# Kernel tuning notes

Hardware: AMD Instinct MI355X
Metric: run time of the kernel (lower is better)

## Reference

```python
import jax, jax.numpy as jnp
import numpy as np

B, T, C = 4, 2048, 1024
NH = 16
HD = C // NH  # 64


def setup_inputs() -> dict:
    key = jax.random.key(0)
    k1, k2, k3, k4, k5 = jax.random.split(key, 5)
    s_in = 1.0 / np.sqrt(C)
    return {
        "x": jax.random.normal(k1, (B, T, C), dtype=jnp.float32),
        "attention_mask": jnp.ones((B, T), dtype=jnp.float32),
        "W_qkv": jax.random.normal(k2, (C, 3 * C), dtype=jnp.float32) * s_in,
        "b_qkv": jnp.zeros((3 * C,), dtype=jnp.float32),
        "W_out": jax.random.normal(k3, (C, C), dtype=jnp.float32) * s_in,
        "b_out": jnp.zeros((C,), dtype=jnp.float32),
    }


def reference(x, attention_mask, W_qkv, b_qkv, W_out, b_out):
    Bx, Tx, Cx = x.shape
    # QKV projection: (B,T,3C)
    qkv = x @ W_qkv + b_qkv
    Q, K, V = jnp.split(qkv, 3, axis=-1)
    # (B, NH, T, HD)
    Q = Q.reshape(Bx, Tx, NH, HD).transpose(0, 2, 1, 3)
    K = K.reshape(Bx, Tx, NH, HD).transpose(0, 2, 1, 3)
    V = V.reshape(Bx, Tx, NH, HD).transpose(0, 2, 1, 3)
    # scaled scores (B, NH, T, T)
    scores = jnp.einsum("bhqd,bhkd->bhqk", Q, K) * (1.0 / np.sqrt(HD))
    # causal mask: set strictly-upper triangle to -inf (mask-fill semantics)
    causal = jnp.tril(jnp.ones((Tx, Tx), dtype=bool))[None, None]
    scores = jnp.where(causal, scores, -jnp.inf)
    # additive padding mask
    pad = (1.0 - attention_mask)[:, None, None, :] * jnp.finfo(scores.dtype).min
    scores = scores + pad
    attn = jax.nn.softmax(scores, axis=-1)
    # weighted values -> (B, T, C)
    wv = jnp.einsum("bhqk,bhkd->bhqd", attn, V)
    wv = wv.transpose(0, 2, 1, 3).reshape(Bx, Tx, Cx)
    return wv @ W_out + b_out
```

## Files before the change

kernel.cpp:

```cpp
#include <hip/hip_runtime.h>
#include <math.h>

constexpr int BB = 4;
constexpr int TT = 2048;
constexpr int CC = 1024;
constexpr int NHH = 16;
constexpr int HDD = 64;
constexpr int C3 = 3 * CC;

typedef __bf16 bf16x8 __attribute__((ext_vector_type(8)));
typedef float  f32x4  __attribute__((ext_vector_type(4)));

__device__ __forceinline__ unsigned short f2bf(float x) {
    union { float f; unsigned u; } v; v.f = x;
    unsigned r = v.u + 0x7fffu + ((v.u >> 16) & 1u);
    return (unsigned short)(r >> 16);
}

#define AS1(p) ((const __attribute__((address_space(1))) void*)(p))
#define AS3(p) ((__attribute__((address_space(3))) void*)(p))

constexpr float SM2 = 17.312340490667561f;

constexpr int CAST_BLOCKS = (BB * TT * CC / 4) / 256;
constexpr int TQKV_BLOCKS = (C3 / 64) * (CC / 64);
constexpr int TOUT_BLOCKS = (CC / 64) * (CC / 64);
constexpr int KB_BLOCKS   = (BB * TT) / 256;

__global__ __launch_bounds__(256) void prep(
    const float* __restrict__ x,
    const float* __restrict__ Wqkv,
    const float* __restrict__ Wout,
    const float* __restrict__ amask,
    unsigned short* __restrict__ xb,
    unsigned short* __restrict__ Wqkvt,
    unsigned short* __restrict__ Woutt,
    float* __restrict__ kbias)
{
    __shared__ float tile[64][65];
    const int bid = blockIdx.x;
    const int t = threadIdx.x;

    if (bid < CAST_BLOCKS) {
        const int i = bid * 256 + t;
        float4 v = ((const float4*)x)[i];
        ushort4 o;
        o.x = f2bf(v.x); o.y = f2bf(v.y); o.z = f2bf(v.z); o.w = f2bf(v.w);
        ((ushort4*)xb)[i] = o;
        return;
    }
    if (bid >= CAST_BLOCKS + TQKV_BLOCKS + TOUT_BLOCKS) {
        const int i = (bid - CAST_BLOCKS - TQKV_BLOCKS - TOUT_BLOCKS) * 256 + t;
        kbias[i] = (amask[i] - 1.0f) * 1.0e38f - SM2;
        return;
    }

    const float* src; unsigned short* dst; int R, Cn, r0, c0;
    if (bid < CAST_BLOCKS + TQKV_BLOCKS) {
        const int tb = bid - CAST_BLOCKS;
        src = Wqkv; dst = Wqkvt; R = CC; Cn = C3;
        c0 = (tb % (C3 / 64)) * 64; r0 = (tb / (C3 / 64)) * 64;
    } else {
        const int tb = bid - CAST_BLOCKS - TQKV_BLOCKS;
        src = Wout; dst = Woutt; R = CC; Cn = CC;
        c0 = (tb % (CC / 64)) * 64; r0 = (tb / (CC / 64)) * 64;
    }

    const int lr = t >> 4, lc = (t & 15) * 4;
    #pragma unroll
    for (int s = 0; s < 4; ++s) {
        float4 v = *(const float4*)&src[(size_t)(r0 + lr + s * 16) * Cn + c0 + lc];
        tile[lr + s * 16][lc + 0] = v.x;
        tile[lr + s * 16][lc + 1] = v.y;
        tile[lr + s * 16][lc + 2] = v.z;
        tile[lr + s * 16][lc + 3] = v.w;
    }
    __syncthreads();
    const int oi = t >> 2, oc = (t & 3) * 16;
    unsigned short buf[16];
    #pragma unroll
    for (int u = 0; u < 16; ++u)
        buf[u] = f2bf(tile[oc + u][oi]);
    unsigned short* d = &dst[(size_t)(c0 + oi) * R + r0 + oc];
    *(uint4*)(d + 0) = *(uint4*)&buf[0];
    *(uint4*)(d + 8) = *(uint4*)&buf[8];
}

template<bool VSPLIT>
__global__ __launch_bounds__(256) void gemm_bt_mfma(
    const unsigned short* __restrict__ A,
    const unsigned short* __restrict__ Bt,
    const float* __restrict__ bias,
    float* __restrict__ OutF,
    unsigned short* __restrict__ Qp,
    unsigned short* __restrict__ Kp,
    unsigned short* __restrict__ Vtp,
    int M, int N, int K, float qscale)
{
    __shared__ alignas(16) unsigned short As[128 * 64];
    __shared__ alignas(16) unsigned short Bs[128 * 64];

    const int tid  = threadIdx.x;
    const int w    = tid >> 6;
    const int lane = tid & 63;
    const int quad = lane >> 4;
    const int col  = lane & 15;
    const int m0 = blockIdx.y * 128, n0 = blockIdx.x * 128;
    const int wr = w >> 1, wc = w & 1;

    f32x4 acc[4][4];
    #pragma unroll
    for (int i = 0; i < 4; ++i)
        #pragma unroll
        for (int j = 0; j < 4; ++j)
            #pragma unroll
            for (int r = 0; r < 4; ++r)
                acc[i][j][r] = 0.0f;

    const int srow = tid >> 3;
    const int spos = tid & 7;
    char* AsB = (char*)As;
    char* BsB = (char*)Bs;

    for (int k0 = 0; k0 < K; k0 += 64) {
        if (k0) __syncthreads();
        #pragma unroll
        for (int i = 0; i < 4; ++i) {
            const int row = srow + 32 * i;
            const int sch = spos ^ (row & 7);
            __builtin_amdgcn_global_load_lds(
                AS1(A + (size_t)(m0 + row) * K + k0 + sch * 8),
                AS3(AsB + i * 4096 + w * 1024), 16, 0, 0);
            __builtin_amdgcn_global_load_lds(
                AS1(Bt + (size_t)(n0 + row) * K + k0 + sch * 8),
                AS3(BsB + i * 4096 + w * 1024), 16, 0, 0);
        }
        __syncthreads();

        #pragma unroll
        for (int ks = 0; ks < 2; ++ks) {
            bf16x8 af[4], bf[4];
            #pragma unroll
            for (int i = 0; i < 4; ++i) {
                const int ra = wr * 64 + i * 16 + col;
                const int pa = ((quad + ks * 4) ^ (ra & 7)) * 8;
                af[i] = *(const bf16x8*)&As[ra * 64 + pa];
                const int rb = wc * 64 + i * 16 + col;
                const int pb = ((quad + ks * 4) ^ (rb & 7)) * 8;
                bf[i] = *(const bf16x8*)&Bs[rb * 64 + pb];
            }
            #pragma unroll
            for (int i = 0; i < 4; ++i)
                #pragma unroll
                for (int j = 0; j < 4; ++j)
                    acc[i][j] = __builtin_amdgcn_mfma_f32_16x16x32_bf16(af[i], bf[j], acc[i][j], 0, 0, 0);
        }
    }

    if (VSPLIT) {
        if (n0 < CC) {
            #pragma unroll
            for (int i = 0; i < 4; ++i)
                #pragma unroll
                for (int r = 0; r < 4; ++r) {
                    const int m = m0 + wr * 64 + i * 16 + quad * 4 + r;
                    #pragma unroll
                    for (int j = 0; j < 4; ++j) {
                        const int n = n0 + wc * 64 + j * 16 + col;
                        Qp[(size_t)m * CC + n] = f2bf((acc[i][j][r] + bias[n]) * qscale);
                    }
                }
        } else if (n0 < 2 * CC) {
            #pragma unroll
            for (int i = 0; i < 4; ++i) {
                const int mb   = m0 + wr * 64 + i * 16 + quad * 4;
                const int bidx = mb >> 11;
                const int tloc = mb & 2047;
                #pragma unroll
                for (int j = 0; j < 4; ++j) {
                    const int n  = n0 + wc * 64 + j * 16 + col;
                    const int hh = (n - CC) >> 6;
                    const int dd = (n - CC) & 63;
                    #pragma unroll
                    for (int r = 0; r < 4; ++r)
                        Kp[(((size_t)bidx * NHH + hh) * TT + tloc + r) * HDD + dd] =
                            f2bf(acc[i][j][r] + bias[n]);
                }
            }
        } else {
            #pragma unroll
            for (int i = 0; i < 4; ++i) {
                const int mb   = m0 + wr * 64 + i * 16 + quad * 4;
                const int bidx = mb >> 11;
                const int tloc = mb & 2047;
                const int ktile = tloc >> 6, tc = tloc & 63;
                #pragma unroll
                for (int j = 0; j < 4; ++j) {
                    const int n  = n0 + wc * 64 + j * 16 + col;
                    const int hh = (n - 2 * CC) >> 6;
                    const int dd = (n - 2 * CC) & 63;
                    unsigned short pk[4];
                    #pragma unroll
                    for (int r = 0; r < 4; ++r)
                        pk[r] = f2bf(acc[i][j][r] + bias[n]);
                    *(uint2*)&Vtp[((((size_t)bidx * NHH + hh) * 32 + ktile) * HDD + dd) * 64 + tc] =
                        *(const uint2*)pk;
                }
            }
        }
    } else {
        #pragma unroll
        for (int i = 0; i < 4; ++i)
            #pragma unroll
            for (int r = 0; r < 4; ++r) {
                const int m = m0 + wr * 64 + i * 16 + quad * 4 + r;
                #pragma unroll
                for (int j = 0; j < 4; ++j) {
                    const int n = n0 + wc * 64 + j * 16 + col;
                    OutF[(size_t)m * N + n] = acc[i][j][r] + bias[n];
                }
            }
    }
}

constexpr int PP = 72;

__global__ __launch_bounds__(256, 2) void attn_mfma(
    const unsigned short* __restrict__ Qp,
    const unsigned short* __restrict__ Kp,
    const unsigned short* __restrict__ Vtp,
    const float* __restrict__ kbias,
    unsigned short* __restrict__ WV)
{
    __shared__ alignas(16) unsigned short Ks [2][64 * 64];
    __shared__ alignas(16) unsigned short Vts[2][64 * 64];
    __shared__ alignas(16) __bf16        Ps[4][32 * PP];

    const int tid  = threadIdx.x;
    const int w    = tid >> 6;
    const int lane = tid & 63;
    const int quad = lane >> 4;
    const int col  = lane & 15;

    const int wid = ((blockIdx.x & 7) << 6) | (blockIdx.x >> 3);
    const int bh = wid >> 3, jx = wid & 7;
    const int b = bh >> 4, h = bh & 15;

    const unsigned short* Qg = Qp + (size_t)b * TT * CC + (size_t)h * HDD;
    const unsigned short* Kg = Kp + (size_t)bh * TT * HDD;
    const unsigned short* Vg = Vtp + (size_t)bh * 32 * HDD * 64;
    const float* kb_g = kbias + b * TT;

    const int srow = tid >> 3;
    const int sch  = (tid & 7) ^ (srow & 7);
    char* KsB  = (char*)&Ks[0][0];
    char* VtsB = (char*)&Vts[0][0];

    #pragma unroll
    for (int ph = 0; ph < 2; ++ph) {
        const int qb    = ph ? (15 - jx) : jx;
        const int qbase = qb * 128;
        const int qw    = qbase + w * 32;

        bf16x8 qfa0 = *(const bf16x8*)(Qg + (size_t)(qw + col) * CC + quad * 8);
        bf16x8 qfa1 = *(const bf16x8*)(Qg + (size_t)(qw + col) * CC + 32 + quad * 8);
        bf16x8 qfb0 = *(const bf16x8*)(Qg + (size_t)(qw + 16 + col) * CC + quad * 8);
        bf16x8 qfb1 = *(const bf16x8*)(Qg + (size_t)(qw + 16 + col) * CC + 32 + quad * 8);

        f32x4 o[2][4];
        float l[2][4];
        #pragma unroll
        for (int hh = 0; hh < 2; ++hh)
            #pragma unroll
            for (int t = 0; t < 4; ++t)
                #pragma unroll
                for (int r = 0; r < 4; ++r) o[hh][t][r] = 0.0f;
        #pragma unroll
        for (int hh = 0; hh < 2; ++hh)
            #pragma unroll
            for (int r = 0; r < 4; ++r) l[hh][r] = 0.0f;

        const int ntiles = 2 * qb + 2;

        #pragma unroll
        for (int i = 0; i < 2; ++i) {
            __builtin_amdgcn_global_load_lds(
                AS1(Kg + (size_t)(srow + 32 * i) * HDD + sch * 8),
                AS3(KsB + i * 4096 + w * 1024), 16, 0, 0);
            __builtin_amdgcn_global_load_lds(
                AS1(Vg + (size_t)(srow + 32 * i) * 64 + sch * 8),
                AS3(VtsB + i * 4096 + w * 1024), 16, 0, 0);
        }
        __syncthreads();

        for (int it = 0; it < ntiles; ++it) {
            const int kt  = it << 6;
            const int cur = it & 1;

            if (it + 1 < ntiles) {
                #pragma unroll
                for (int i = 0; i < 2; ++i) {
                    __builtin_amdgcn_global_load_lds(
                        AS1(Kg + (size_t)(kt + 64 + srow + 32 * i) * HDD + sch * 8),
                        AS3(KsB + (cur ^ 1) * 8192 + i * 4096 + w * 1024), 16, 0, 0);
                    __builtin_amdgcn_global_load_lds(
                        AS1(Vg + ((size_t)(it + 1) * 64 + srow + 32 * i) * 64 + sch * 8),
                        AS3(VtsB + (cur ^ 1) * 8192 + i * 4096 + w * 1024), 16, 0, 0);
                }
            }

            if (kt <= qw + 31) {
                const unsigned short* ksb = &Ks[cur][0];
                const unsigned short* vsb = &Vts[cur][0];

                float kb[4];
                #pragma unroll
                for (int t = 0; t < 4; ++t)
                    kb[t] = kb_g[kt + t * 16 + col];

                f32x4 s[2][4];
                #pragma unroll
                for (int t = 0; t < 4; ++t) {
                    const int row = t * 16 + col;
                    const int c0 = (quad ^ (row & 7)) * 8;
                    const int c1 = ((quad + 4) ^ (row & 7)) * 8;
                    bf16x8 k0 = *(const bf16x8*)&ksb[row * 64 + c0];
                    bf16x8 k1 = *(const bf16x8*)&ksb[row * 64 + c1];
                    f32x4 z;
                    #pragma unroll
                    for (int r = 0; r < 4; ++r) z[r] = kb[t];
                    f32x4 za = __builtin_amdgcn_mfma_f32_16x16x32_bf16(qfa0, k0, z, 0, 0, 0);
                    za = __builtin_amdgcn_mfma_f32_16x16x32_bf16(qfa1, k1, za, 0, 0, 0);
                    s[0][t] = za;
                    f32x4 zb = __builtin_amdgcn_mfma_f32_16x16x32_bf16(qfb0, k0, z, 0, 0, 0);
                    zb = __builtin_amdgcn_mfma_f32_16x16x32_bf16(qfb1, k1, zb, 0, 0, 0);
                    s[1][t] = zb;
                }

                const bool needc = (kt + 64 > qw);
                #pragma unroll
                for (int hh = 0; hh < 2; ++hh)
                    #pragma unroll
                    for (int t = 0; t < 4; ++t) {
                        const int key = kt + t * 16 + col;
                        #pragma unroll
                        for (int r = 0; r < 4; ++r) {
                            float p = __builtin_amdgcn_exp2f(s[hh][t][r]);
                            if (needc && key > qw + hh * 16 + quad * 4 + r) p = 0.0f;
                            l[hh][r] += p;
                            Ps[w][(hh * 16 + quad * 4 + r) * PP + t * 16 + col] = (__bf16)p;
                        }
                    }

                bf16x8 p0a = *(const bf16x8*)&Ps[w][col * PP + quad * 8];
                bf16x8 p1a = *(const bf16x8*)&Ps[w][col * PP + 32 + quad * 8];
                bf16x8 p0b = *(const bf16x8*)&Ps[w][(16 + col) * PP + quad * 8];
                bf16x8 p1b = *(const bf16x8*)&Ps[w][(16 + col) * PP + 32 + quad * 8];
                #pragma unroll
                for (int t = 0; t < 4; ++t) {
                    const int row = t * 16 + col;
                    const int c0 = (quad ^ (row & 7)) * 8;
                    const int c1 = ((quad + 4) ^ (row & 7)) * 8;
                    bf16x8 v0 = *(const bf16x8*)&vsb[row * 64 + c0];
                    bf16x8 v1 = *(const bf16x8*)&vsb[row * 64 + c1];
                    o[0][t] = __builtin_amdgcn_mfma_f32_16x16x32_bf16(p0a, v0, o[0][t], 0, 0, 0);
                    o[0][t] = __builtin_amdgcn_mfma_f32_16x16x32_bf16(p1a, v1, o[0][t], 0, 0, 0);
                    o[1][t] = __builtin_amdgcn_mfma_f32_16x16x32_bf16(p0b, v0, o[1][t], 0, 0, 0);
                    o[1][t] = __builtin_amdgcn_mfma_f32_16x16x32_bf16(p1b, v1, o[1][t], 0, 0, 0);
                }
            }
            __syncthreads();
        }

        #pragma unroll
        for (int hh = 0; hh < 2; ++hh) {
            #pragma unroll
            for (int off = 1; off < 16; off <<= 1)
                #pragma unroll
                for (int r = 0; r < 4; ++r)
                    l[hh][r] += __shfl_xor(l[hh][r], off);
            #pragma unroll
            for (int r = 0; r < 4; ++r) {
                const float inv = 1.0f / l[hh][r];
                const int q = qw + hh * 16 + quad * 4 + r;
                unsigned short* dst = WV + ((size_t)b * TT + q) * CC + (size_t)h * HDD;
                #pragma unroll
                for (int t = 0; t < 4; ++t)
                    dst[t * 16 + col] = f2bf(o[hh][t][r] * inv);
            }
        }
    }
}

extern "C" void kernel_launch(void* const* d_in, const int* in_sizes, int n_in,
                              void* d_out, int out_size, void* d_ws, size_t ws_size,
                              hipStream_t stream) {
    const float* x     = (const float*)d_in[0];
    const float* amask = (const float*)d_in[1];
    const float* Wqkv  = (const float*)d_in[2];
    const float* bqkv  = (const float*)d_in[3];
    const float* Wout  = (const float*)d_in[4];
    const float* bout  = (const float*)d_in[5];
    float* out = (float*)d_out;

    const int M = BB * TT;

    unsigned short* xb    = (unsigned short*)d_ws;
    unsigned short* Wqkvt = xb    + (size_t)M * CC;
    unsigned short* Woutt = Wqkvt + (size_t)C3 * CC;
    unsigned short* Qp    = Woutt + (size_t)CC * CC;
    unsigned short* Kp    = Qp    + (size_t)M * CC;
    unsigned short* Vtp   = Kp    + (size_t)M * CC;
    unsigned short* wvb   = Vtp   + (size_t)M * CC;
    float*          kbias = (float*)(wvb + (size_t)M * CC);

    dim3 blk(256);

    prep<<<dim3(CAST_BLOCKS + TQKV_BLOCKS + TOUT_BLOCKS + KB_BLOCKS), blk, 0, stream>>>(
        x, Wqkv, Wout, amask, xb, Wqkvt, Woutt, kbias);

    gemm_bt_mfma<true><<<dim3(C3 / 128, M / 128), blk, 0, stream>>>(
        xb, Wqkvt, bqkv, nullptr, Qp, Kp, Vtp, M, C3, CC, 0.18033688011112043f);
    attn_mfma<<<dim3(512), dim3(256), 0, stream>>>(
        Qp, Kp, Vtp, kbias, wvb);
    gemm_bt_mfma<false><<<dim3(CC / 128, M / 128), blk, 0, stream>>>(
        wvb, Woutt, bout, out, nullptr, nullptr, nullptr, M, CC, CC, 1.0f);
}
```

Before: 257.2 us.

## Split attention into one query block per CTA with depth-2 DMA prefetch

The attention kernel no longer pairs two causal query blocks (jx and 15-jx) per block. It launches 1024 blocks, one query block each, ordered longest-first so the heavy blocks are scheduled early and load balance comes from the hardware scheduler. The K/V pipeline now keeps two tiles in flight, using explicit vmcnt waits and raw s_barrier in place of __syncthreads, and it prefetches key-bias values a tile ahead. Launch bounds are raised to 3 blocks per SM to allow more occupancy. The risks are register pressure at the tighter bound and the hand-written waitcnt counts, which must match the number of DMA and bias loads issued per tile.

```diff
diff --git a/kernel.cpp b/kernel.cpp
--- a/kernel.cpp
+++ b/kernel.cpp
@@ -225,7 +225,7 @@
 
 constexpr int PP = 72;
 
-__global__ __launch_bounds__(256, 2) void attn_mfma(
+__global__ __launch_bounds__(256, 3) void attn_mfma(
     const unsigned short* __restrict__ Qp,
     const unsigned short* __restrict__ Kp,
     const unsigned short* __restrict__ Vtp,
@@ -242,8 +242,10 @@
     const int quad = lane >> 4;
     const int col  = lane & 15;
 
-    const int wid = ((blockIdx.x & 7) << 6) | (blockIdx.x >> 3);
-    const int bh = wid >> 3, jx = wid & 7;
+    const int gi = blockIdx.x;
+    const int j  = gi >> 3;
+    const int bh = ((gi & 7) << 3) | (j & 7);
+    const int qb = 15 - (j >> 3);
     const int b = bh >> 4, h = bh & 15;
 
     const unsigned short* Qg = Qp + (size_t)b * TT * CC + (size_t)h * HDD;
@@ -256,138 +258,141 @@
     char* KsB  = (char*)&Ks[0][0];
     char* VtsB = (char*)&Vts[0][0];
 
-    #pragma unroll
-    for (int ph = 0; ph < 2; ++ph) {
-        const int qb    = ph ? (15 - jx) : jx;
-        const int qbase = qb * 128;
-        const int qw    = qbase + w * 32;
-
-        bf16x8 qfa0 = *(const bf16x8*)(Qg + (size_t)(qw + col) * CC + quad * 8);
-        bf16x8 qfa1 = *(const bf16x8*)(Qg + (size_t)(qw + col) * CC + 32 + quad * 8);
-        bf16x8 qfb0 = *(const bf16x8*)(Qg + (size_t)(qw + 16 + col) * CC + quad * 8);
-        bf16x8 qfb1 = *(const bf16x8*)(Qg + (size_t)(qw + 16 + col) * CC + 32 + quad * 8);
-
-        f32x4 o[2][4];
-        float l[2][4];
-        #pragma unroll
-        for (int hh = 0; hh < 2; ++hh)
-            #pragma unroll
-            for (int t = 0; t < 4; ++t)
-                #pragma unroll
-                for (int r = 0; r < 4; ++r) o[hh][t][r] = 0.0f;
-        #pragma unroll
-        for (int hh = 0; hh < 2; ++hh)
-            #pragma unroll
-            for (int r = 0; r < 4; ++r) l[hh][r] = 0.0f;
-
-        const int ntiles = 2 * qb + 2;
-
+    const int qw = qb * 128 + w * 32;
+    const int ntiles = 2 * qb + 2;
+
+    bf16x8 qfa0 = *(const bf16x8*)(Qg + (size_t)(qw + col) * CC + quad * 8);
+    bf16x8 qfa1 = *(const bf16x8*)(Qg + (size_t)(qw + col) * CC + 32 + quad * 8);
+    bf16x8 qfb0 = *(const bf16x8*)(Qg + (size_t)(qw + 16 + col) * CC + quad * 8);
+    bf16x8 qfb1 = *(const bf16x8*)(Qg + (size_t)(qw + 16 + col) * CC + 32 + quad * 8);
+
+    f32x4 o[2][4];
+    float l[2][4];
+    #pragma unroll
+    for (int hh = 0; hh < 2; ++hh)
+        #pragma unroll
+        for (int t = 0; t < 4; ++t)
+            #pragma unroll
+            for (int r = 0; r < 4; ++r) o[hh][t][r] = 0.0f;
+    #pragma unroll
+    for (int hh = 0; hh < 2; ++hh)
+        #pragma unroll
+        for (int r = 0; r < 4; ++r) l[hh][r] = 0.0f;
+
+    auto DMA = [&](int tile, int buf) {
         #pragma unroll
         for (int i = 0; i < 2; ++i) {
             __builtin_amdgcn_global_load_lds(
-                AS1(Kg + (size_t)(srow + 32 * i) * HDD + sch * 8),
-                AS3(KsB + i * 4096 + w * 1024), 16, 0, 0);
+                AS1(Kg + (size_t)(tile * 64 + srow + 32 * i) * HDD + sch * 8),
+                AS3(KsB + buf * 8192 + i * 4096 + w * 1024), 16, 0, 0);
             __builtin_amdgcn_global_load_lds(
-                AS1(Vg + (size_t)(srow + 32 * i) * 64 + sch * 8),
-                AS3(VtsB + i * 4096 + w * 1024), 16, 0, 0);
-        }
-        __syncthreads();
-
-        for (int it = 0; it < ntiles; ++it) {
-            const int kt  = it << 6;
-            const int cur = it & 1;
-
-            if (it + 1 < ntiles) {
-                #pragma unroll
-                for (int i = 0; i < 2; ++i) {
-                    __builtin_amdgcn_global_load_lds(
-                        AS1(Kg + (size_t)(kt + 64 + srow + 32 * i) * HDD + sch * 8),
-                        AS3(KsB + (cur ^ 1) * 8192 + i * 4096 + w * 1024), 16, 0, 0);
-                    __builtin_amdgcn_global_load_lds(
-                        AS1(Vg + ((size_t)(it + 1) * 64 + srow + 32 * i) * 64 + sch * 8),
-                        AS3(VtsB + (cur ^ 1) * 8192 + i * 4096 + w * 1024), 16, 0, 0);
+                AS1(Vg + ((size_t)tile * 64 + srow + 32 * i) * 64 + sch * 8),
+                AS3(VtsB + buf * 8192 + i * 4096 + w * 1024), 16, 0, 0);
+        }
+    };
+
+    float kbc[4], kbn[4];
+    DMA(0, 0);
+    #pragma unroll
+    for (int t = 0; t < 4; ++t) kbc[t] = kb_g[t * 16 + col];
+    DMA(1, 1);
+    #pragma unroll
+    for (int t = 0; t < 4; ++t) kbn[t] = kb_g[64 + t * 16 + col];
+    asm volatile("s_waitcnt vmcnt(8)" ::: "memory");
+    __builtin_amdgcn_s_barrier();
+
+    for (int it = 0; it < ntiles; ++it) {
+        const int kt  = it << 6;
+        const int cur = it & 1;
+
+        if (kt <= qw + 31) {
+            const unsigned short* ksb = &Ks[cur][0];
+            const unsigned short* vsb = &Vts[cur][0];
+
+            f32x4 s[2][4];
+            #pragma unroll
+            for (int t = 0; t < 4; ++t) {
+                const int row = t * 16 + col;
+                const int c0 = (quad ^ (row & 7)) * 8;
+                const int c1 = ((quad + 4) ^ (row & 7)) * 8;
+                bf16x8 k0 = *(const bf16x8*)&ksb[row * 64 + c0];
+                bf16x8 k1 = *(const bf16x8*)&ksb[row * 64 + c1];
+                f32x4 z;
+                #pragma unroll
+                for (int r = 0; r < 4; ++r) z[r] = kbc[t];
+                f32x4 za = __builtin_amdgcn_mfma_f32_16x16x32_bf16(qfa0, k0, z, 0, 0, 0);
+                za = __builtin_amdgcn_mfma_f32_16x16x32_bf16(qfa1, k1, za, 0, 0, 0);
+                s[0][t] = za;
+                f32x4 zb = __builtin_amdgcn_mfma_f32_16x16x32_bf16(qfb0, k0, z, 0, 0, 0);
+                zb = __builtin_amdgcn_mfma_f32_16x16x32_bf16(qfb1, k1, zb, 0, 0, 0);
+                s[1][t] = zb;
+            }
+
+            const bool needc = (kt + 64 > qw);
+            #pragma unroll
+            for (int hh = 0; hh < 2; ++hh)
+                #pragma unroll
+                for (int t = 0; t < 4; ++t) {
+                    const int key = kt + t * 16 + col;
+                    #pragma unroll
+                    for (int r = 0; r < 4; ++r) {
+                        float p = __builtin_amdgcn_exp2f(s[hh][t][r]);
+                        if (needc && key > qw + hh * 16 + quad * 4 + r) p = 0.0f;
+                        l[hh][r] += p;
+                        Ps[w][(hh * 16 + quad * 4 + r) * PP + t * 16 + col] = (__bf16)p;
+                    }
                 }
-            }
-
-            if (kt <= qw + 31) {
-                const unsigned short* ksb = &Ks[cur][0];
-                const unsigned short* vsb = &Vts[cur][0];
-
-                float kb[4];
-                #pragma unroll
-                for (int t = 0; t < 4; ++t)
-                    kb[t] = kb_g[kt + t * 16 + col];
-
-                f32x4 s[2][4];
-                #pragma unroll
-                for (int t = 0; t < 4; ++t) {
-                    const int row = t * 16 + col;
-                    const int c0 = (quad ^ (row & 7)) * 8;
-                    const int c1 = ((quad + 4) ^ (row & 7)) * 8;
-                    bf16x8 k0 = *(const bf16x8*)&ksb[row * 64 + c0];
-                    bf16x8 k1 = *(const bf16x8*)&ksb[row * 64 + c1];
-                    f32x4 z;
-                    #pragma unroll
-                    for (int r = 0; r < 4; ++r) z[r] = kb[t];
-                    f32x4 za = __builtin_amdgcn_mfma_f32_16x16x32_bf16(qfa0, k0, z, 0, 0, 0);
-                    za = __builtin_amdgcn_mfma_f32_16x16x32_bf16(qfa1, k1, za, 0, 0, 0);
-                    s[0][t] = za;
-                    f32x4 zb = __builtin_amdgcn_mfma_f32_16x16x32_bf16(qfb0, k0, z, 0, 0, 0);
-                    zb = __builtin_amdgcn_mfma_f32_16x16x32_bf16(qfb1, k1, zb, 0, 0, 0);
-                    s[1][t] = zb;
-                }
-
-                const bool needc = (kt + 64 > qw);
-                #pragma unroll
-                for (int hh = 0; hh < 2; ++hh)
-                    #pragma unroll
-                    for (int t = 0; t < 4; ++t) {
-                        const int key = kt + t * 16 + col;
-                        #pragma unroll
-                        for (int r = 0; r < 4; ++r) {
-                            float p = __builtin_amdgcn_exp2f(s[hh][t][r]);
-                            if (needc && key > qw + hh * 16 + quad * 4 + r) p = 0.0f;
-                            l[hh][r] += p;
-                            Ps[w][(hh * 16 + quad * 4 + r) * PP + t * 16 + col] = (__bf16)p;
-                        }
-                    }
-
-                bf16x8 p0a = *(const bf16x8*)&Ps[w][col * PP + quad * 8];
-                bf16x8 p1a = *(const bf16x8*)&Ps[w][col * PP + 32 + quad * 8];
-                bf16x8 p0b = *(const bf16x8*)&Ps[w][(16 + col) * PP + quad * 8];
-                bf16x8 p1b = *(const bf16x8*)&Ps[w][(16 + col) * PP + 32 + quad * 8];
-                #pragma unroll
-                for (int t = 0; t < 4; ++t) {
-                    const int row = t * 16 + col;
-                    const int c0 = (quad ^ (row & 7)) * 8;
-                    const int c1 = ((quad + 4) ^ (row & 7)) * 8;
-                    bf16x8 v0 = *(const bf16x8*)&vsb[row * 64 + c0];
-                    bf16x8 v1 = *(const bf16x8*)&vsb[row * 64 + c1];
-                    o[0][t] = __builtin_amdgcn_mfma_f32_16x16x32_bf16(p0a, v0, o[0][t], 0, 0, 0);
-                    o[0][t] = __builtin_amdgcn_mfma_f32_16x16x32_bf16(p1a, v1, o[0][t], 0, 0, 0);
-                    o[1][t] = __builtin_amdgcn_mfma_f32_16x16x32_bf16(p0b, v0, o[1][t], 0, 0, 0);
-                    o[1][t] = __builtin_amdgcn_mfma_f32_16x16x32_bf16(p1b, v1, o[1][t], 0, 0, 0);
-                }
-            }
-            __syncthreads();
-        }
-
-        #pragma unroll
-        for (int hh = 0; hh < 2; ++hh) {
-            #pragma unroll
-            for (int off = 1; off < 16; off <<= 1)
-                #pragma unroll
-                for (int r = 0; r < 4; ++r)
-                    l[hh][r] += __shfl_xor(l[hh][r], off);
-            #pragma unroll
-            for (int r = 0; r < 4; ++r) {
-                const float inv = 1.0f / l[hh][r];
-                const int q = qw + hh * 16 + quad * 4 + r;
-                unsigned short* dst = WV + ((size_t)b * TT + q) * CC + (size_t)h * HDD;
-                #pragma unroll
-                for (int t = 0; t < 4; ++t)
-                    dst[t * 16 + col] = f2bf(o[hh][t][r] * inv);
-            }
+
+            bf16x8 p0a = *(const bf16x8*)&Ps[w][col * PP + quad * 8];
+            bf16x8 p1a = *(const bf16x8*)&Ps[w][col * PP + 32 + quad * 8];
+            bf16x8 p0b = *(const bf16x8*)&Ps[w][(16 + col) * PP + quad * 8];
+            bf16x8 p1b = *(const bf16x8*)&Ps[w][(16 + col) * PP + 32 + quad * 8];
+            #pragma unroll
+            for (int t = 0; t < 4; ++t) {
+                const int row = t * 16 + col;
+                const int c0 = (quad ^ (row & 7)) * 8;
+                const int c1 = ((quad + 4) ^ (row & 7)) * 8;
+                bf16x8 v0 = *(const bf16x8*)&vsb[row * 64 + c0];
+                bf16x8 v1 = *(const bf16x8*)&vsb[row * 64 + c1];
+                o[0][t] = __builtin_amdgcn_mfma_f32_16x16x32_bf16(p0a, v0, o[0][t], 0, 0, 0);
+                o[0][t] = __builtin_amdgcn_mfma_f32_16x16x32_bf16(p1a, v1, o[0][t], 0, 0, 0);
+                o[1][t] = __builtin_amdgcn_mfma_f32_16x16x32_bf16(p0b, v0, o[1][t], 0, 0, 0);
+                o[1][t] = __builtin_amdgcn_mfma_f32_16x16x32_bf16(p1b, v1, o[1][t], 0, 0, 0);
+            }
+        }
+
+        __builtin_amdgcn_s_barrier();
+
+        #pragma unroll
+        for (int t = 0; t < 4; ++t) kbc[t] = kbn[t];
+
+        if (it + 2 < ntiles) {
+            DMA(it + 2, cur);
+            #pragma unroll
+            for (int t = 0; t < 4; ++t)
+                kbn[t] = kb_g[(it + 2) * 64 + t * 16 + col];
+            asm volatile("s_waitcnt vmcnt(8)" ::: "memory");
+        } else {
+            asm volatile("s_waitcnt vmcnt(0)" ::: "memory");
+        }
+        __builtin_amdgcn_s_barrier();
+    }
+
+    #pragma unroll
+    for (int hh = 0; hh < 2; ++hh) {
+        #pragma unroll
+        for (int off = 1; off < 16; off <<= 1)
+            #pragma unroll
+            for (int r = 0; r < 4; ++r)
+                l[hh][r] += __shfl_xor(l[hh][r], off);
+        #pragma unroll
+        for (int r = 0; r < 4; ++r) {
+            const float inv = 1.0f / l[hh][r];
+            const int q = qw + hh * 16 + quad * 4 + r;
+            unsigned short* dst = WV + ((size_t)b * TT + q) * CC + (size_t)h * HDD;
+            #pragma unroll
+            for (int t = 0; t < 4; ++t)
+                dst[t * 16 + col] = f2bf(o[hh][t][r] * inv);
         }
     }
 }
@@ -421,7 +426,7 @@
 
     gemm_bt_mfma<true><<<dim3(C3 / 128, M / 128), blk, 0, stream>>>(
         xb, Wqkvt, bqkv, nullptr, Qp, Kp, Vtp, M, C3, CC, 0.18033688011112043f);
-    attn_mfma<<<dim3(512), dim3(256), 0, stream>>>(
+    attn_mfma<<<dim3(1024), dim3(256), 0, stream>>>(
         Qp, Kp, Vtp, kbias, wvb);
     gemm_bt_mfma<false><<<dim3(CC / 128, M / 128), blk, 0, stream>>>(
         wvb, Woutt, bout, out, nullptr, nullptr, nullptr, M, CC, CC, 1.0f);
```

New measurement: 243.7 us. 1.06x faster.
